# Performance work log

Hardware: AMD Instinct MI355X
Metric: run time of the kernel (lower is better)

Reference implementation:

```python
import jax, jax.numpy as jnp
import numpy as np

S = 2        # scale
KUP = 5      # k_up
EPS = 1e-5   # BatchNorm eps


def _conv(x, w, p):
    return jax.lax.conv_general_dilated(
        x, w, (1, 1), [(p, p), (p, p)],
        dimension_numbers=('NCHW', 'OIHW', 'NCHW'))


def _bn(x, g, b, m, v):
    sc = g * jax.lax.rsqrt(v + EPS)
    return x * sc[None, :, None, None] + (b - m * sc)[None, :, None, None]


def setup_inputs() -> dict:
    key = jax.random.key(0)
    ks = jax.random.split(key, 11)
    c, c_mid = 256, 64
    return {
        'X': jax.random.normal(ks[0], (2, c, 48, 48), jnp.float32),
        'w_comp': jax.random.normal(ks[1], (c_mid, c, 1, 1), jnp.float32) * 0.05,
        'g1': jax.random.uniform(ks[2], (c_mid,), jnp.float32, 0.5, 1.5),
        'b1': jax.random.normal(ks[3], (c_mid,), jnp.float32) * 0.1,
        'm1': jax.random.normal(ks[4], (c_mid,), jnp.float32) * 0.1,
        'v1': jax.random.uniform(ks[5], (c_mid,), jnp.float32, 0.5, 1.5),
        'w_enc': jax.random.normal(ks[6], (100, c_mid, 3, 3), jnp.float32) * 0.05,
        'g2': jax.random.uniform(ks[7], (100,), jnp.float32, 0.5, 1.5),
        'b2': jax.random.normal(ks[8], (100,), jnp.float32) * 0.1,
        'm2': jax.random.normal(ks[9], (100,), jnp.float32) * 0.1,
        'v2': jax.random.uniform(ks[10], (100,), jnp.float32, 0.5, 1.5),
    }


def reference(X, w_comp, g1, b1, m1, v1, w_enc, g2, b2, m2, v2):
    b, c, h, w = X.shape
    h_, w_ = h * S, w * S
    k2 = KUP * KUP
    # comp: 1x1 conv + BN + SiLU
    t = _bn(_conv(X, w_comp, 0), g1, b1, m1, v1)
    t = t * jax.nn.sigmoid(t)
    # enc: 3x3 conv + BN (no act) -> (b, (S*KUP)^2, h, w)
    e = _bn(_conv(t, w_enc, 1), g2, b2, m2, v2)
    # PixelShuffle(S): (b, k2*S*S, h, w) -> (b, k2, h*S, w*S)
    e = e.reshape(b, k2, S, S, h, w).transpose(0, 1, 4, 2, 5, 3).reshape(b, k2, h_, w_)
    Wk = jax.nn.softmax(e, axis=1)  # per-pixel reassembly weights over k_up^2 taps
    # nearest-neighbor upsample by S
    Xup = jnp.repeat(jnp.repeat(X, S, axis=2), S, axis=3)
    # Unfold(kernel=KUP, dilation=S, padding=(KUP//2)*S): spatial size preserved
    pad = (KUP // 2) * S
    xp = jnp.pad(Xup, ((0, 0), (0, 0), (pad, pad), (pad, pad)))
    # taps in row-major (ky, kx) order, matching torch Unfold + view(b,c,k2,h_,w_)
    patches = jnp.stack(
        [xp[:, :, i * S:i * S + h_, j * S:j * S + w_]
         for i in range(KUP) for j in range(KUP)], axis=2)  # (b, c, k2, h_, w_)
    return jnp.einsum('bkhw,bckhw->bchw', Wk, patches)
```

## Files before the change

kernel.cpp:

```cpp
#include <hip/hip_runtime.h>

#define EPS_BN 1e-5f

typedef __attribute__((ext_vector_type(8))) short short8v;
typedef __attribute__((ext_vector_type(4))) float f32x4;

__device__ inline unsigned short f2bf(float f) {
    union { float f; unsigned u; } v; v.f = f;
    unsigned r = v.u + 0x7fffu + ((v.u >> 16) & 1u);
    return (unsigned short)(r >> 16);
}

__global__ __launch_bounds__(256) void prep_kernel(
    const float* __restrict__ w_enc, const float* __restrict__ w_comp,
    uint4* __restrict__ tpad_v, unsigned short* __restrict__ Web,
    unsigned short* __restrict__ Wcb)
{
    const int tid = blockIdx.x * 256 + threadIdx.x;
    const int nthr = gridDim.x * 256;
    const uint4 z = {0u,0u,0u,0u};
    for (int i = tid; i < 40000; i += nthr)
        tpad_v[i] = z;
    for (int i = tid; i < 128 * 576; i += nthr) {
        int ch = i / 576;
        int r  = i - ch * 576;
        int kk = r >> 6;
        int ci = r & 63;
        float v = (ch < 100) ? w_enc[ch * 576 + ci * 9 + kk] : 0.f;
        Web[i] = f2bf(v);
    }
    for (int i = tid; i < 64 * 256; i += nthr)
        Wcb[i] = f2bf(w_comp[i]);
}

__global__ __launch_bounds__(256) void comp_mfma(
    const float* __restrict__ X, const unsigned short* __restrict__ Wcb,
    const float* __restrict__ g1, const float* __restrict__ b1,
    const float* __restrict__ m1, const float* __restrict__ v1,
    unsigned short* __restrict__ tpad)
{
    const int wseg = blockIdx.x;
    const int h = blockIdx.y;
    const int b = blockIdx.z;
    const int tid  = threadIdx.x;
    const int wave = tid >> 6;
    const int l    = tid & 63;
    const int lr   = l & 15;
    const int lk   = l >> 4;
    const int w0   = wseg * 16;

    f32x4 acc = {0.f,0.f,0.f,0.f};
    const float* xb = X + (size_t)b * 589824 + h * 48 + w0 + lr;
    const unsigned short* wb = Wcb + (wave * 16 + lr) * 256;

    #pragma unroll
    for (int s = 0; s < 8; ++s) {
        const int ci0 = s * 32 + lk * 8;
        short8v a;
        #pragma unroll
        for (int j = 0; j < 8; ++j)
            a[j] = (short)f2bf(xb[(size_t)(ci0 + j) * 2304]);
        const short8v f = *(const short8v*)(wb + ci0);
        acc = __builtin_amdgcn_mfma_f32_16x16x32_bf16(a, f, acc, 0, 0, 0);
    }

    const int oc = wave * 16 + lr;
    const float sc = g1[oc] * rsqrtf(v1[oc] + EPS_BN);
    const float sh = b1[oc] - m1[oc] * sc;
    unsigned short* tp = tpad + ((b*50 + h + 1)*50 + 1)*64 + oc;
    #pragma unroll
    for (int r = 0; r < 4; ++r) {
        float v = fmaf(acc[r], sc, sh);
        float t = v / (1.f + __expf(-v));
        tp[(w0 + lk*4 + r)*64] = f2bf(t);
    }
}

__global__ __launch_bounds__(256) void enc_sm(
    const unsigned short* __restrict__ tpad, const unsigned short* __restrict__ Web,
    const float* __restrict__ g2, const float* __restrict__ b2,
    const float* __restrict__ m2, const float* __restrict__ v2,
    float* __restrict__ Wl)
{
    const int wseg = blockIdx.x;
    const int h = blockIdx.y;
    const int b = blockIdx.z;
    const int tid  = threadIdx.x;
    const int wave = tid >> 6;
    const int l    = tid & 63;
    const int lr   = l & 15;
    const int lk   = l >> 4;
    const int w0   = wseg * 16;
    const int nt0  = wave * 2, nt1 = wave * 2 + 1;
    __shared__ float elds[16 * 116];

    f32x4 acc0 = {0.f,0.f,0.f,0.f};
    f32x4 acc1 = {0.f,0.f,0.f,0.f};

    const unsigned short* tb = tpad + (b*50 + h)*50*64;
    const unsigned short* wb0 = Web + (nt0*16 + lr)*576;
    const unsigned short* wb1 = Web + (nt1*16 + lr)*576;

    #pragma unroll 6
    for (int s = 0; s < 18; ++s) {
        const int kk = s >> 1;
        const int ky = (kk * 11) >> 5;
        const int kx = kk - ky * 3;
        const int cio = ((s & 1) << 5) + lk * 8;
        const short8v a  = *(const short8v*)(tb + (ky*50 + w0 + kx + lr)*64 + cio);
        const short8v f0 = *(const short8v*)(wb0 + kk*64 + cio);
        const short8v f1 = *(const short8v*)(wb1 + kk*64 + cio);
        acc0 = __builtin_amdgcn_mfma_f32_16x16x32_bf16(a, f0, acc0, 0, 0, 0);
        acc1 = __builtin_amdgcn_mfma_f32_16x16x32_bf16(a, f1, acc1, 0, 0, 0);
    }

    #pragma unroll
    for (int t = 0; t < 2; ++t) {
        const int nt = t ? nt1 : nt0;
        if (nt >= 7) continue;
        const int ch = nt*16 + lr;
        float sc = 0.f, sh = 0.f;
        if (ch < 100) {
            sc = g2[ch] * rsqrtf(v2[ch] + EPS_BN);
            sh = b2[ch] - m2[ch]*sc;
        }
        const f32x4 acc = t ? acc1 : acc0;
        #pragma unroll
        for (int r = 0; r < 4; ++r)
            elds[(lk*4 + r)*116 + ch] = fmaf(acc[r], sc, sh);
    }
    __syncthreads();

    if (tid < 64) {
        const int px = tid >> 2;
        const int s  = tid & 3;
        const float* ep = &elds[px*116 + s];
        float ev[25];
        float mx = -1e30f;
        #pragma unroll
        for (int k = 0; k < 25; ++k) { ev[k] = ep[4*k]; mx = fmaxf(mx, ev[k]); }
        float sum = 0.f;
        #pragma unroll
        for (int k = 0; k < 25; ++k) { ev[k] = __expf(ev[k] - mx); sum += ev[k]; }
        const float rs = 1.f / sum;
        float* wp = Wl + ((b*48 + h)*48 + w0 + px)*112 + s*28;
        #pragma unroll
        for (int k4 = 0; k4 < 6; ++k4) {
            float4 o = { ev[k4*4+0]*rs, ev[k4*4+1]*rs, ev[k4*4+2]*rs, ev[k4*4+3]*rs };
            *(float4*)(wp + k4*4) = o;
        }
        wp[24] = ev[24]*rs;
    }
}

__global__ __launch_bounds__(256) void carafe_v6(
    const float* __restrict__ X, const float* __restrict__ Wl,
    float* __restrict__ out)
{
    const int cg = blockIdx.x;
    const int h = blockIdx.y;
    const int b = blockIdx.z;
    __shared__ float xl[4240];
    const int tid = threadIdx.x;

    for (int idx = tid; idx < 960; idx += 256) {
        const int ci  = idx / 60;
        const int rem = idx - ci * 60;
        const int r   = rem / 12;
        const int q   = rem - r * 12;
        const int hh  = h - 2 + r;
        float4 v = {0.f,0.f,0.f,0.f};
        if ((unsigned)hh < 48u)
            v = *(const float4*)&X[(size_t)(b*256 + cg*16 + ci)*2304 + hh*48 + q*4];
        float* base = &xl[(((ci>>2)*5 + r)*53 + 2 + q*4)*4 + (ci&3)];
        base[0]  = v.x;
        base[4]  = v.y;
        base[8]  = v.z;
        base[12] = v.w;
    }
    for (int idx = tid; idx < 320; idx += 256) {
        const int ci  = idx / 20;
        const int rem = idx - ci * 20;
        const int r   = rem / 4;
        const int e   = rem & 3;
        const int cp  = (e < 2) ? e : 48 + e;
        xl[(((ci>>2)*5 + r)*53 + cp)*4 + (ci&3)] = 0.f;
    }
    __syncthreads();

    const int c4g = tid & 3;
    const int w   = tid >> 2;
    if (w < 48) {
        float4 xv[25];
        #pragma unroll
        for (int r = 0; r < 5; ++r)
            #pragma unroll
            for (int dx = 0; dx < 5; ++dx)
                xv[r*5 + dx] = *(const float4*)&xl[((c4g*5 + r)*53 + (w + dx))*4];
        const float* wb = &Wl[(size_t)((b*48 + h)*48 + w)*112];
        #pragma unroll
        for (int s = 0; s < 4; ++s) {
            float ax=0.f, ay=0.f, az=0.f, aw=0.f;
            #pragma unroll
            for (int k4 = 0; k4 < 6; ++k4) {
                const float4 wv = *(const float4*)&wb[s*28 + k4*4];
                const float4 p0 = xv[k4*4+0], p1 = xv[k4*4+1], p2 = xv[k4*4+2], p3 = xv[k4*4+3];
                ax = fmaf(wv.x,p0.x,fmaf(wv.y,p1.x,fmaf(wv.z,p2.x,fmaf(wv.w,p3.x,ax))));
                ay = fmaf(wv.x,p0.y,fmaf(wv.y,p1.y,fmaf(wv.z,p2.y,fmaf(wv.w,p3.y,ay))));
                az = fmaf(wv.x,p0.z,fmaf(wv.y,p1.z,fmaf(wv.z,p2.z,fmaf(wv.w,p3.z,az))));
                aw = fmaf(wv.x,p0.w,fmaf(wv.y,p1.w,fmaf(wv.z,p2.w,fmaf(wv.w,p3.w,aw))));
            }
            const float wk = wb[s*28 + 24];
            const float4 pl = xv[24];
            ax = fmaf(wk,pl.x,ax); ay = fmaf(wk,pl.y,ay);
            az = fmaf(wk,pl.z,az); aw = fmaf(wk,pl.w,aw);
            const int y = 2*h + (s>>1);
            const int x = 2*w + (s&1);
            float* ob = &out[((size_t)(b*256 + cg*16 + c4g*4)*96 + y)*96 + x];
            ob[0]     = ax;
            ob[9216]  = ay;
            ob[18432] = az;
            ob[27648] = aw;
        }
    }
}

extern "C" void kernel_launch(void* const* d_in, const int* in_sizes, int n_in,
                              void* d_out, int out_size, void* d_ws, size_t ws_size,
                              hipStream_t stream)
{
    (void)in_sizes; (void)n_in; (void)out_size; (void)ws_size;
    const float* X      = (const float*)d_in[0];
    const float* w_comp = (const float*)d_in[1];
    const float* g1     = (const float*)d_in[2];
    const float* b1     = (const float*)d_in[3];
    const float* m1     = (const float*)d_in[4];
    const float* v1     = (const float*)d_in[5];
    const float* w_enc  = (const float*)d_in[6];
    const float* g2     = (const float*)d_in[7];
    const float* b2     = (const float*)d_in[8];
    const float* m2     = (const float*)d_in[9];
    const float* v2     = (const float*)d_in[10];
    float* out = (float*)d_out;

    char* ws = (char*)d_ws;
    unsigned short* tpad = (unsigned short*)(ws + 0);
    unsigned short* Web  = (unsigned short*)(ws + 640000);
    unsigned short* Wcb  = (unsigned short*)(ws + 787456);
    float*          Wl   = (float*)(ws + 820224);

    prep_kernel<<<128, 256, 0, stream>>>(w_enc, w_comp, (uint4*)tpad, Web, Wcb);
    dim3 gA(3, 48, 2);
    comp_mfma<<<gA, 256, 0, stream>>>(X, Wcb, g1, b1, m1, v1, tpad);
    dim3 gB(3, 48, 2);
    enc_sm<<<gB, 256, 0, stream>>>(tpad, Web, g2, b2, m2, v2, Wl);
    dim3 gC(16, 48, 2);
    carafe_v6<<<gC, 256, 0, stream>>>(X, Wl, out);
}
```

Baseline: 46.23 us.

## Fold weight prep into comp kernel and stage carafe output through LDS

Removes the separate prep kernel. Its work moves into comp_mfma: each thread converts one w_enc element to bf16, and the threads with i < 25088 zero only the padding border of tpad instead of the whole buffer. comp_mfma now reads the fp32 w_comp weights directly and converts them to bf16 in registers. The carafe kernel now writes its results into shared memory first and then stores them to global memory as coalesced float4 rows, replacing the strided scalar stores. This saves one launch and a lot of memory traffic, at the cost of an extra barrier and redundant weight conversion in every comp block.

```diff
diff --git a/kernel.cpp b/kernel.cpp
--- a/kernel.cpp
+++ b/kernel.cpp
@@ -11,38 +11,40 @@
     return (unsigned short)(r >> 16);
 }
 
-__global__ __launch_bounds__(256) void prep_kernel(
-    const float* __restrict__ w_enc, const float* __restrict__ w_comp,
-    uint4* __restrict__ tpad_v, unsigned short* __restrict__ Web,
-    unsigned short* __restrict__ Wcb)
-{
-    const int tid = blockIdx.x * 256 + threadIdx.x;
-    const int nthr = gridDim.x * 256;
-    const uint4 z = {0u,0u,0u,0u};
-    for (int i = tid; i < 40000; i += nthr)
-        tpad_v[i] = z;
-    for (int i = tid; i < 128 * 576; i += nthr) {
-        int ch = i / 576;
-        int r  = i - ch * 576;
-        int kk = r >> 6;
-        int ci = r & 63;
-        float v = (ch < 100) ? w_enc[ch * 576 + ci * 9 + kk] : 0.f;
-        Web[i] = f2bf(v);
-    }
-    for (int i = tid; i < 64 * 256; i += nthr)
-        Wcb[i] = f2bf(w_comp[i]);
-}
-
 __global__ __launch_bounds__(256) void comp_mfma(
-    const float* __restrict__ X, const unsigned short* __restrict__ Wcb,
+    const float* __restrict__ X, const float* __restrict__ w_comp,
+    const float* __restrict__ w_enc,
     const float* __restrict__ g1, const float* __restrict__ b1,
     const float* __restrict__ m1, const float* __restrict__ v1,
-    unsigned short* __restrict__ tpad)
+    unsigned short* __restrict__ tpad, unsigned short* __restrict__ Web)
 {
     const int wseg = blockIdx.x;
     const int h = blockIdx.y;
     const int b = blockIdx.z;
     const int tid  = threadIdx.x;
+
+    {
+        const int i = ((wseg + 3*(h + 48*b)) << 8) | tid;
+        const int ch = i / 576;
+        const int r  = i - ch * 576;
+        const int kk = r >> 6;
+        const int ci = r & 63;
+        const float v = (ch < 100) ? w_enc[ch * 576 + ci * 9 + kk] : 0.f;
+        Web[i] = f2bf(v);
+        if (i < 25088) {
+            const int bb  = i / 12544;
+            const int rem = i - bb * 12544;
+            const int p   = rem >> 6;
+            const int chn = rem & 63;
+            int rr, cc;
+            if (p < 50)       { rr = 0;       cc = p;       }
+            else if (p < 100) { rr = 49;      cc = p - 50;  }
+            else if (p < 148) { rr = p - 99;  cc = 0;       }
+            else              { rr = p - 147; cc = 49;      }
+            tpad[((bb*50 + rr)*50 + cc)*64 + chn] = 0;
+        }
+    }
+
     const int wave = tid >> 6;
     const int l    = tid & 63;
     const int lr   = l & 15;
@@ -51,16 +53,21 @@
 
     f32x4 acc = {0.f,0.f,0.f,0.f};
     const float* xb = X + (size_t)b * 589824 + h * 48 + w0 + lr;
-    const unsigned short* wb = Wcb + (wave * 16 + lr) * 256;
+    const float* wb = w_comp + (wave * 16 + lr) * 256;
 
     #pragma unroll
     for (int s = 0; s < 8; ++s) {
         const int ci0 = s * 32 + lk * 8;
-        short8v a;
+        short8v a, f;
+        const float4 wv0 = *(const float4*)(wb + ci0);
+        const float4 wv1 = *(const float4*)(wb + ci0 + 4);
+        f[0] = (short)f2bf(wv0.x); f[1] = (short)f2bf(wv0.y);
+        f[2] = (short)f2bf(wv0.z); f[3] = (short)f2bf(wv0.w);
+        f[4] = (short)f2bf(wv1.x); f[5] = (short)f2bf(wv1.y);
+        f[6] = (short)f2bf(wv1.z); f[7] = (short)f2bf(wv1.w);
         #pragma unroll
         for (int j = 0; j < 8; ++j)
             a[j] = (short)f2bf(xb[(size_t)(ci0 + j) * 2304]);
-        const short8v f = *(const short8v*)(wb + ci0);
         acc = __builtin_amdgcn_mfma_f32_16x16x32_bf16(a, f, acc, 0, 0, 0);
     }
 
@@ -153,7 +160,7 @@
     }
 }
 
-__global__ __launch_bounds__(256) void carafe_v6(
+__global__ __launch_bounds__(256) void carafe_v8(
     const float* __restrict__ X, const float* __restrict__ Wl,
     float* __restrict__ out)
 {
@@ -190,13 +197,19 @@
 
     const int c4g = tid & 3;
     const int w   = tid >> 2;
+
+    float4 xv[25];
     if (w < 48) {
-        float4 xv[25];
         #pragma unroll
         for (int r = 0; r < 5; ++r)
             #pragma unroll
             for (int dx = 0; dx < 5; ++dx)
                 xv[r*5 + dx] = *(const float4*)&xl[((c4g*5 + r)*53 + (w + dx))*4];
+    }
+    __syncthreads();
+
+    float* ol = xl;
+    if (w < 48) {
         const float* wb = &Wl[(size_t)((b*48 + h)*48 + w)*112];
         #pragma unroll
         for (int s = 0; s < 4; ++s) {
@@ -214,14 +227,25 @@
             const float4 pl = xv[24];
             ax = fmaf(wk,pl.x,ax); ay = fmaf(wk,pl.y,ay);
             az = fmaf(wk,pl.z,az); aw = fmaf(wk,pl.w,aw);
-            const int y = 2*h + (s>>1);
-            const int x = 2*w + (s&1);
-            float* ob = &out[((size_t)(b*256 + cg*16 + c4g*4)*96 + y)*96 + x];
-            ob[0]     = ax;
-            ob[9216]  = ay;
-            ob[18432] = az;
-            ob[27648] = aw;
-        }
+            const int y = s >> 1;
+            const int x = 2*w + (s & 1);
+            ol[((c4g*4 + 0)*2 + y)*96 + x] = ax;
+            ol[((c4g*4 + 1)*2 + y)*96 + x] = ay;
+            ol[((c4g*4 + 2)*2 + y)*96 + x] = az;
+            ol[((c4g*4 + 3)*2 + y)*96 + x] = aw;
+        }
+    }
+    __syncthreads();
+
+    #pragma unroll
+    for (int p = 0; p < 3; ++p) {
+        const int fi = p*256 + tid;
+        const int ch = fi / 48;
+        const int rem = fi - ch*48;
+        const int y  = rem / 24;
+        const int xq = rem - y*24;
+        const float4 v = *(const float4*)&ol[fi*4];
+        *(float4*)&out[((size_t)(b*256 + cg*16 + ch)*96 + 2*h + y)*96 + xq*4] = v;
     }
 }
 
@@ -246,14 +270,12 @@
     char* ws = (char*)d_ws;
     unsigned short* tpad = (unsigned short*)(ws + 0);
     unsigned short* Web  = (unsigned short*)(ws + 640000);
-    unsigned short* Wcb  = (unsigned short*)(ws + 787456);
-    float*          Wl   = (float*)(ws + 820224);
-
-    prep_kernel<<<128, 256, 0, stream>>>(w_enc, w_comp, (uint4*)tpad, Web, Wcb);
+    float*          Wl   = (float*)(ws + 787456);
+
     dim3 gA(3, 48, 2);
-    comp_mfma<<<gA, 256, 0, stream>>>(X, Wcb, g1, b1, m1, v1, tpad);
+    comp_mfma<<<gA, 256, 0, stream>>>(X, w_comp, w_enc, g1, b1, m1, v1, tpad, Web);
     dim3 gB(3, 48, 2);
     enc_sm<<<gB, 256, 0, stream>>>(tpad, Web, g2, b2, m2, v2, Wl);
     dim3 gC(16, 48, 2);
-    carafe_v6<<<gC, 256, 0, stream>>>(X, Wl, out);
-}
+    carafe_v8<<<gC, 256, 0, stream>>>(X, Wl, out);
+}
```

Result: faster. 43.43 us (-6.0%).
